# Performance work log

Hardware: AMD Instinct MI355X
Metric: run time of the kernel (lower is better)

The kernel has to match this reference:

```python
import jax, jax.numpy as jnp
import numpy as np

B, S, HID, HEADS = 1, 2048, 4096, 32
HEAD_D = HID // HEADS
SCALE = float(1.0 / np.sqrt(HEAD_D))  # = 1/norm_factor^2 with use_mup=False


def setup_inputs() -> dict:
    key = jax.random.key(0)
    k0, k1, k2, k3, k4 = jax.random.split(key, 5)
    return {
        "x": jax.random.normal(k0, (B, S, HID), jnp.float32),
        "attn_qkvw": jax.random.normal(k1, (HID, 3 * HID), jnp.float32) * 0.02,
        "attn_qkvb": jax.random.normal(k2, (3 * HID,), jnp.float32) * 0.02,
        "attn_ow": jax.random.normal(k3, (HID, HID), jnp.float32) * 0.02,
        "attn_ob": jax.random.normal(k4, (HID,), jnp.float32) * 0.02,
    }


def reference(x, attn_qkvw, attn_qkvb, attn_ow, attn_ob):
    # QKV projection (LinearOp): [B,S,HID] @ [HID,3*HID] + bias -> packed qkv
    qkv = x @ attn_qkvw + attn_qkvb
    q, k, v = jnp.split(qkv, 3, axis=-1)  # each [B,S,HID]

    def to_heads(t):
        return t.reshape(B, S, HEADS, HEAD_D)

    q, k, v = to_heads(q), to_heads(k), to_heads(v)
    # flash kernel math: softmax(scale * q k^T + causal mask) @ v (numerically
    # stable online softmax == standard stable softmax)
    scores = jnp.einsum("bqhd,bkhd->bhqk", q, k) * jnp.float32(SCALE)
    causal = jnp.tril(jnp.ones((S, S), dtype=bool))  # P_SEQ = 0
    scores = jnp.where(causal[None, None], scores, jnp.float32(-jnp.inf))
    attn = jax.nn.softmax(scores, axis=-1)
    ctx = jnp.einsum("bhqk,bkhd->bqhd", attn, v).reshape(B, S, HID)
    # output projection
    return ctx @ attn_ow + attn_ob
```

## Files before the change

kernel.cpp:

```cpp
#include <hip/hip_runtime.h>
#include <hip/hip_bf16.h>
#include <math.h>

typedef __bf16 bf16_t;
typedef __bf16 bf16x8 __attribute__((ext_vector_type(8)));
typedef float f32x4 __attribute__((ext_vector_type(4)));

#define AS1 __attribute__((address_space(1)))
#define AS3 __attribute__((address_space(3)))

static constexpr int S_  = 2048;
static constexpr int HID = 4096;
static constexpr int NH  = 32;
static constexpr int HD  = 128;
static constexpr int N3  = 3 * HID;
static constexpr float SC2 = 0.12751674581f;
static constexpr float THR = 11.0f;

__global__ void cvt_f32_bf16(const float* __restrict__ in, bf16_t* __restrict__ out, int n4) {
  int i = blockIdx.x * blockDim.x + threadIdx.x;
  if (i >= n4) return;
  float4 v = ((const float4*)in)[i];
  union { bf16_t h[4]; short4 s4; } u;
  u.h[0] = (bf16_t)v.x; u.h[1] = (bf16_t)v.y; u.h[2] = (bf16_t)v.z; u.h[3] = (bf16_t)v.w;
  ((short4*)out)[i] = u.s4;
}

__global__ __launch_bounds__(256) void transcvt64(
    const float* __restrict__ in, bf16_t* __restrict__ out, int R, int C) {
  __shared__ float t[64][65];
  const int r0 = blockIdx.y * 64, c0 = blockIdx.x * 64;
  const int tid = threadIdx.x;
  const int rr = tid >> 4, c4 = (tid & 15) * 4;
#pragma unroll
  for (int it = 0; it < 4; ++it) {
    float4 v = *(const float4*)&in[(size_t)(r0 + rr + it * 16) * C + c0 + c4];
    t[rr + it * 16][c4 + 0] = v.x;
    t[rr + it * 16][c4 + 1] = v.y;
    t[rr + it * 16][c4 + 2] = v.z;
    t[rr + it * 16][c4 + 3] = v.w;
  }
  __syncthreads();
  const int cc = tid >> 3, r8 = (tid & 7) * 8;
#pragma unroll
  for (int it = 0; it < 2; ++it) {
    const int c = cc + it * 32;
    bf16x8 w;
#pragma unroll
    for (int j = 0; j < 8; ++j) w[j] = (bf16_t)t[r8 + j][c];
    *(bf16x8*)&out[(size_t)(c0 + c) * R + r0 + r8] = w;
  }
}

__global__ void vtrans(const bf16_t* __restrict__ qkv, bf16_t* __restrict__ vt) {
  __shared__ bf16_t t[32][33];
  int h = blockIdx.z;
  int s0 = blockIdx.x * 32, d0 = blockIdx.y * 32;
  int tx = threadIdx.x, ty = threadIdx.y;
#pragma unroll
  for (int i = 0; i < 32; i += 8)
    t[ty + i][tx] = qkv[(size_t)(s0 + ty + i) * N3 + 2 * HID + h * HD + d0 + tx];
  __syncthreads();
#pragma unroll
  for (int i = 0; i < 32; i += 8)
    vt[(size_t)(h * HD + d0 + ty + i) * S_ + s0 + tx] = t[tx][ty + i];
}

template <bool STG, int VMC>
__device__ __forceinline__ void wstep(
    const char* slot, int aoff, int boff,
    const bf16_t* gA, const bf16_t* gB, int kst, size_t row64,
    char* stgA, char* stgB, f32x4 (&acc)[8][4]) {
  bf16x8 a[8], b[4];
#pragma unroll
  for (int mi = 0; mi < 8; ++mi) a[mi] = *(const bf16x8*)(slot + aoff + mi * 1024);
#pragma unroll
  for (int ni = 0; ni < 4; ++ni) b[ni] = *(const bf16x8*)(slot + 16384 + boff + ni * 1024);
  if constexpr (STG) {
#pragma unroll
    for (int i = 0; i < 4; ++i)
      __builtin_amdgcn_global_load_lds((const AS1 void*)(gA + i * row64 + kst),
                                       (AS3 void*)(stgA + i * 4096), 16, 0, 0);
#pragma unroll
    for (int j = 0; j < 2; ++j)
      __builtin_amdgcn_global_load_lds((const AS1 void*)(gB + j * row64 + kst),
                                       (AS3 void*)(stgB + j * 4096), 16, 0, 0);
  }
  if constexpr (VMC == 6)      asm volatile("s_waitcnt vmcnt(6)" ::: "memory");
  else if constexpr (VMC == 0) asm volatile("s_waitcnt vmcnt(0)" ::: "memory");
  asm volatile("s_waitcnt lgkmcnt(0)" ::: "memory");
  __builtin_amdgcn_s_barrier();
  __builtin_amdgcn_s_setprio(1);
#pragma unroll
  for (int mi = 0; mi < 8; ++mi)
#pragma unroll
    for (int ni = 0; ni < 4; ++ni)
      acc[mi][ni] = __builtin_amdgcn_mfma_f32_16x16x32_bf16(a[mi], b[ni], acc[mi][ni], 0, 0, 0);
  __builtin_amdgcn_s_setprio(0);
}

__global__ __launch_bounds__(256, 2) void gemm_w(
    const bf16_t* __restrict__ A, const bf16_t* __restrict__ BT,
    const float* __restrict__ bias, bf16_t* __restrict__ C,
    int M, int N, int K, int ntiles) {
  extern __shared__ char smem[];
  const int tid = threadIdx.x;
  const int wv = tid >> 6, ln = tid & 63;
  const int lr = ln & 15, lg = ln >> 4;
  const int wm = wv >> 1, wn = wv & 1;

  const int nx = N >> 7;
  const int chunk = ntiles >> 3;

  const int lrow = wv * 16 + (ln >> 2);
  const int lcol = ((ln & 3) << 3) ^ ((ln & 32) >> 1);
  const size_t row64 = (size_t)64 * K;
  const int sw = (lr & 8) << 2;
  const int aoff = (wm * 128 + lr) * 64 + ((lg * 16) ^ sw);
  const int boff = (wn * 64 + lr) * 64 + ((lg * 16) ^ sw);
  const int NT = K >> 5;

  for (int tt = blockIdx.x; tt < ntiles; tt += gridDim.x) {
    const int wg = (tt & 7) * chunk + (tt >> 3);
    const int m0 = (wg / nx) * 256, n0 = (wg % nx) * 128;

    const bf16_t* gA = A + (size_t)(m0 + lrow) * K + lcol;
    const bf16_t* gB = BT + (size_t)(n0 + lrow) * K + lcol;

    f32x4 acc[8][4] = {};

#pragma unroll
    for (int t = 0; t < 2; ++t) {
      char* dA = smem + t * 24576 + wv * 1024;
      char* dB = dA + 16384;
#pragma unroll
      for (int i = 0; i < 4; ++i)
        __builtin_amdgcn_global_load_lds((const AS1 void*)(gA + i * row64 + t * 32),
                                         (AS3 void*)(dA + i * 4096), 16, 0, 0);
#pragma unroll
      for (int j = 0; j < 2; ++j)
        __builtin_amdgcn_global_load_lds((const AS1 void*)(gB + j * row64 + t * 32),
                                         (AS3 void*)(dB + j * 4096), 16, 0, 0);
    }
    asm volatile("s_waitcnt vmcnt(6)" ::: "memory");
    __builtin_amdgcn_s_barrier();

    int slot = 0, nslot = 2;
    int t = 0;
    for (; t < NT - 2; ++t) {
      char* sb = smem + nslot * 24576 + wv * 1024;
      wstep<true, 6>(smem + slot * 24576, aoff, boff, gA, gB, (t + 2) * 32,
                     row64, sb, sb + 16384, acc);
      slot = (slot == 2) ? 0 : slot + 1;
      nslot = (nslot == 2) ? 0 : nslot + 1;
    }
    wstep<false, 0>(smem + slot * 24576, aoff, boff, gA, gB, 0, row64, smem, smem, acc);
    slot = (slot == 2) ? 0 : slot + 1;
    wstep<false, -1>(smem + slot * 24576, aoff, boff, gA, gB, 0, row64, smem, smem, acc);

#pragma unroll
    for (int mi = 0; mi < 8; ++mi)
#pragma unroll
      for (int ni = 0; ni < 4; ++ni) {
        const int col = n0 + wn * 64 + ni * 16 + lr;
        const float bv = bias[col];
#pragma unroll
        for (int i = 0; i < 4; ++i) {
          const int row = m0 + wm * 128 + mi * 16 + lg * 4 + i;
          C[(size_t)row * N + col] = (bf16_t)(acc[mi][ni][i] + bv);
        }
      }
  }
}

template <bool STG, int VMC>
__device__ __forceinline__ void tile_step(
    const char* slot, int aoff, int boff,
    const bf16_t* gA, const bf16_t* gB, int kst, size_t skA,
    char* stg_dst, f32x4 (&acc)[4][4]) {
  bf16x8 a[4], b[4];
#pragma unroll
  for (int mi = 0; mi < 4; ++mi) a[mi] = *(const bf16x8*)(slot + aoff + mi * 1024);
#pragma unroll
  for (int ni = 0; ni < 4; ++ni) b[ni] = *(const bf16x8*)(slot + 16384 + boff + ni * 1024);
  if constexpr (STG) {
    __builtin_amdgcn_global_load_lds((const AS1 void*)(gA + kst), (AS3 void*)(stg_dst), 16, 0, 0);
    __builtin_amdgcn_global_load_lds((const AS1 void*)(gA + skA + kst), (AS3 void*)(stg_dst + 8192), 16, 0, 0);
    __builtin_amdgcn_global_load_lds((const AS1 void*)(gB + kst), (AS3 void*)(stg_dst + 16384), 16, 0, 0);
  }
  if constexpr (VMC == 3)      asm volatile("s_waitcnt vmcnt(3)" ::: "memory");
  else if constexpr (VMC == 0) asm volatile("s_waitcnt vmcnt(0)" ::: "memory");
  asm volatile("s_waitcnt lgkmcnt(0)" ::: "memory");
  __builtin_amdgcn_s_barrier();
  __builtin_amdgcn_s_setprio(1);
#pragma unroll
  for (int mi = 0; mi < 4; ++mi)
#pragma unroll
    for (int ni = 0; ni < 4; ++ni)
      acc[mi][ni] = __builtin_amdgcn_mfma_f32_16x16x32_bf16(a[mi], b[ni], acc[mi][ni], 0, 0, 0);
  __builtin_amdgcn_s_setprio(0);
}

template <typename OutT>
__global__ __launch_bounds__(512, 4) void gemm_p(
    const bf16_t* __restrict__ A, const bf16_t* __restrict__ BT,
    const float* __restrict__ bias, OutT* __restrict__ C,
    int M, int N, int K, int ntiles) {
  extern __shared__ char smem[];
  const int tid = threadIdx.x;
  const int wv = tid >> 6, ln = tid & 63;
  const int lr = ln & 15, lg = ln >> 4;
  const int wm = wv >> 1, wn = wv & 1;

  const int nx = N >> 7;
  const int chunk = ntiles >> 3;

  const int lrow = wv * 16 + (ln >> 2);
  const int lcol = ((ln & 3) << 3) ^ ((ln & 32) >> 1);
  const size_t skA = (size_t)128 * K;
  const int sw = (lr & 8) << 2;
  const int aoff = (wm * 64 + lr) * 64 + ((lg * 16) ^ sw);
  const int boff = (wn * 64 + lr) * 64 + ((lg * 16) ^ sw);
  const int NT = K >> 5;

  for (int tt = blockIdx.x; tt < ntiles; tt += gridDim.x) {
    const int wg = (tt & 7) * chunk + (tt >> 3);
    const int m0 = (wg / nx) * 256, n0 = (wg % nx) * 128;

    const bf16_t* gA = A + (size_t)(m0 + lrow) * K + lcol;
    const bf16_t* gB = BT + (size_t)(n0 + lrow) * K + lcol;

    f32x4 acc[4][4] = {};

#pragma unroll
    for (int t = 0; t < 2; ++t) {
      char* d = smem + t * 24576 + wv * 1024;
      __builtin_amdgcn_global_load_lds((const AS1 void*)(gA + t * 32), (AS3 void*)(d), 16, 0, 0);
      __builtin_amdgcn_global_load_lds((const AS1 void*)(gA + skA + t * 32), (AS3 void*)(d + 8192), 16, 0, 0);
      __builtin_amdgcn_global_load_lds((const AS1 void*)(gB + t * 32), (AS3 void*)(d + 16384), 16, 0, 0);
    }
    asm volatile("s_waitcnt vmcnt(3)" ::: "memory");
    __builtin_amdgcn_s_barrier();

    int slot = 0, nslot = 2;
    int t = 0;
    for (; t < NT - 2; ++t) {
      tile_step<true, 3>(smem + slot * 24576, aoff, boff, gA, gB, (t + 2) * 32,
                         skA, smem + nslot * 24576 + wv * 1024, acc);
      slot = (slot == 2) ? 0 : slot + 1;
      nslot = (nslot == 2) ? 0 : nslot + 1;
    }
    tile_step<false, 0>(smem + slot * 24576, aoff, boff, gA, gB, 0, skA, smem, acc);
    slot = (slot == 2) ? 0 : slot + 1;
    tile_step<false, -1>(smem + slot * 24576, aoff, boff, gA, gB, 0, skA, smem, acc);

#pragma unroll
    for (int mi = 0; mi < 4; ++mi)
#pragma unroll
      for (int ni = 0; ni < 4; ++ni) {
        const int col = n0 + wn * 64 + ni * 16 + lr;
        const float bv = bias[col];
#pragma unroll
        for (int i = 0; i < 4; ++i) {
          const int row = m0 + wm * 64 + mi * 16 + lg * 4 + i;
          C[(size_t)row * N + col] = (OutT)(acc[mi][ni][i] + bv);
        }
      }
  }
}

__global__ __launch_bounds__(256, 2) void attn_fwd(
    const bf16_t* __restrict__ qkv, const bf16_t* __restrict__ vt,
    bf16_t* __restrict__ ctx) {
  __shared__ __align__(16) bf16_t Ks[64][136];
  __shared__ __align__(16) bf16_t Vts[128][72];

  const int tid = threadIdx.x;
  const int wv = tid >> 6, ln = tid & 63;
  bf16_t* Pl = &Ks[0][0] + wv * (32 * 68);

  const int bid = blockIdx.x;
  const int a = bid >> 3;
  const int hsub = a >> 4;
  const int h  = ((bid & 7) << 2) + hsub;
  const int qt = 15 - (((a & 15) + (hsub << 2)) & 15);
  const int q0 = qt * 128;
  const int lr = ln & 15, lg = ln >> 4;
  const int rbase = q0 + 32 * wv;

  bf16x8 qf[2][4];
#pragma unroll
  for (int rg = 0; rg < 2; ++rg)
#pragma unroll
    for (int kk = 0; kk < 4; ++kk) {
      bf16x8 r = *(const bf16x8*)(qkv + (size_t)(rbase + 16 * rg + lr) * N3 + h * HD + kk * 32 + lg * 8);
#pragma unroll
      for (int j = 0; j < 8; ++j) r[j] = (bf16_t)((float)r[j] * SC2);
      qf[rg][kk] = r;
    }

  f32x4 oacc[2][8] = {};
  float mrow[2][4], psum[2][4];
#pragma unroll
  for (int rg = 0; rg < 2; ++rg)
#pragma unroll
    for (int i = 0; i < 4; ++i) { mrow[rg][i] = -INFINITY; psum[rg][i] = 0.f; }

  const int k_r = tid >> 4, k_c = (tid & 15) * 8;
  const int v_r = tid >> 3, v_c = (tid & 7) * 8;
  bf16x8 kr[4], vr[4];

#pragma unroll
  for (int it = 0; it < 4; ++it) {
    kr[it] = *(const bf16x8*)(qkv + (size_t)(k_r + it * 16) * N3 + HID + h * HD + k_c);
    vr[it] = *(const bf16x8*)(vt + (size_t)(h * HD + v_r + it * 32) * S_ + v_c);
  }

  const int ntiles = 2 * qt + 2;
  for (int t = 0; t < ntiles; ++t) {
    const int kv0 = t * 64;
    const int kvn = (t + 1 < ntiles) ? kv0 + 64 : 0;
    __syncthreads();
#pragma unroll
    for (int it = 0; it < 4; ++it) {
      *(bf16x8*)&Ks[k_r + it * 16][k_c] = kr[it];
      *(bf16x8*)&Vts[v_r + it * 32][v_c] = vr[it];
    }
#pragma unroll
    for (int it = 0; it < 4; ++it) {
      kr[it] = *(const bf16x8*)(qkv + (size_t)(kvn + k_r + it * 16) * N3 + HID + h * HD + k_c);
      vr[it] = *(const bf16x8*)(vt + (size_t)(h * HD + v_r + it * 32) * S_ + kvn + v_c);
    }
    __syncthreads();

    f32x4 sacc[2][4] = {};
#pragma unroll
    for (int kk = 0; kk < 4; ++kk)
#pragma unroll
      for (int ni = 0; ni < 4; ++ni) {
        bf16x8 kf = *(const bf16x8*)&Ks[16 * ni + lr][kk * 32 + lg * 8];
        sacc[0][ni] = __builtin_amdgcn_mfma_f32_16x16x32_bf16(qf[0][kk], kf, sacc[0][ni], 0, 0, 0);
        sacc[1][ni] = __builtin_amdgcn_mfma_f32_16x16x32_bf16(qf[1][kk], kf, sacc[1][ni], 0, 0, 0);
      }

    float p[2][4][4];
    float mx[2][4];
    bool grow = false;
#pragma unroll
    for (int rg = 0; rg < 2; ++rg) {
      const bool needmask = (kv0 + 63 > rbase + 16 * rg);
#pragma unroll
      for (int i = 0; i < 4; ++i) {
        const int row = rbase + 16 * rg + lg * 4 + i;
        float m_ = -INFINITY;
#pragma unroll
        for (int ni = 0; ni < 4; ++ni) {
          float s = sacc[rg][ni][i];
          if (needmask && (kv0 + 16 * ni + lr > row)) s = -INFINITY;
          p[rg][ni][i] = s;
          m_ = fmaxf(m_, s);
        }
        m_ = fmaxf(m_, __shfl_xor(m_, 1, 64));
        m_ = fmaxf(m_, __shfl_xor(m_, 2, 64));
        m_ = fmaxf(m_, __shfl_xor(m_, 4, 64));
        m_ = fmaxf(m_, __shfl_xor(m_, 8, 64));
        mx[rg][i] = m_;
        grow |= (m_ > mrow[rg][i] + THR);
      }
    }
    if (__any(grow)) {
#pragma unroll
      for (int rg = 0; rg < 2; ++rg) {
        float alpha[4];
#pragma unroll
        for (int i = 0; i < 4; ++i) {
          const float mn = fmaxf(mrow[rg][i], mx[rg][i]);
          alpha[i] = exp2f(mrow[rg][i] - mn);
          mrow[rg][i] = mn;
          psum[rg][i] *= alpha[i];
        }
#pragma unroll
        for (int nf = 0; nf < 8; ++nf)
#pragma unroll
          for (int i = 0; i < 4; ++i) oacc[rg][nf][i] *= alpha[i];
      }
    }
#pragma unroll
    for (int rg = 0; rg < 2; ++rg)
#pragma unroll
      for (int i = 0; i < 4; ++i) {
        float ps = 0.f;
#pragma unroll
        for (int ni = 0; ni < 4; ++ni) {
          float e = exp2f(p[rg][ni][i] - mrow[rg][i]);
          p[rg][ni][i] = e;
          ps += e;
        }
        psum[rg][i] += ps;
      }

    __syncthreads();

#pragma unroll
    for (int rg = 0; rg < 2; ++rg)
#pragma unroll
      for (int ni = 0; ni < 4; ++ni)
#pragma unroll
        for (int i = 0; i < 4; ++i)
          Pl[(16 * rg + lg * 4 + i) * 68 + 16 * ni + lr] = (bf16_t)p[rg][ni][i];

#pragma unroll
    for (int kk2 = 0; kk2 < 2; ++kk2) {
      bf16x8 pf0 = *(const bf16x8*)&Pl[lr * 68 + kk2 * 32 + lg * 8];
      bf16x8 pf1 = *(const bf16x8*)&Pl[(16 + lr) * 68 + kk2 * 32 + lg * 8];
#pragma unroll
      for (int nf = 0; nf < 8; ++nf) {
        bf16x8 vf = *(const bf16x8*)&Vts[16 * nf + lr][kk2 * 32 + lg * 8];
        oacc[0][nf] = __builtin_amdgcn_mfma_f32_16x16x32_bf16(pf0, vf, oacc[0][nf], 0, 0, 0);
        oacc[1][nf] = __builtin_amdgcn_mfma_f32_16x16x32_bf16(pf1, vf, oacc[1][nf], 0, 0, 0);
      }
    }
  }

#pragma unroll
  for (int rg = 0; rg < 2; ++rg) {
#pragma unroll
    for (int i = 0; i < 4; ++i) {
      float s = psum[rg][i];
      s += __shfl_xor(s, 1, 64);
      s += __shfl_xor(s, 2, 64);
      s += __shfl_xor(s, 4, 64);
      s += __shfl_xor(s, 8, 64);
      psum[rg][i] = 1.f / s;
    }
#pragma unroll
    for (int nf = 0; nf < 8; ++nf)
#pragma unroll
      for (int i = 0; i < 4; ++i) {
        int row = rbase + 16 * rg + lg * 4 + i;
        int col = h * HD + 16 * nf + lr;
        ctx[(size_t)row * HID + col] = (bf16_t)(oacc[rg][nf][i] * psum[rg][i]);
      }
  }
}

extern "C" void kernel_launch(void* const* d_in, const int* in_sizes, int n_in,
                              void* d_out, int out_size, void* d_ws, size_t ws_size,
                              hipStream_t stream) {
  const float* x    = (const float*)d_in[0];
  const float* wqkv = (const float*)d_in[1];
  const float* bqkv = (const float*)d_in[2];
  const float* ow   = (const float*)d_in[3];
  const float* ob   = (const float*)d_in[4];
  float* out = (float*)d_out;

  char* w = (char*)d_ws;
  bf16_t* xb    = (bf16_t*)(w);
  bf16_t* wqkvT = (bf16_t*)(w + (size_t)16777216);
  bf16_t* qkv   = (bf16_t*)(w + (size_t)117440512);
  bf16_t* vt    = (bf16_t*)(w + (size_t)167772160);
  bf16_t* ctx   = (bf16_t*)(w + (size_t)184549376);
  bf16_t* owT   = (bf16_t*)(w + (size_t)201326592);

  (void)in_sizes; (void)n_in; (void)out_size; (void)ws_size;

  cvt_f32_bf16<<<(S_ * HID / 4 + 255) / 256, 256, 0, stream>>>(x, xb, S_ * HID / 4);
  transcvt64<<<dim3(N3 / 64, HID / 64), 256, 0, stream>>>(wqkv, wqkvT, HID, N3);
  transcvt64<<<dim3(HID / 64, HID / 64), 256, 0, stream>>>(ow, owT, HID, HID);
  gemm_w<<<512, 256, 73728, stream>>>(xb, wqkvT, bqkv, qkv, S_, N3, HID,
                                      (S_ / 256) * (N3 / 128));
  vtrans<<<dim3(S_ / 32, HD / 32, NH), dim3(32, 8), 0, stream>>>(qkv, vt);
  attn_fwd<<<(S_ / 128) * NH, 256, 0, stream>>>(qkv, vt, ctx);
  gemm_p<float><<<256, 512, 73728, stream>>>(ctx, owT, ob, out, S_, HID, HID,
                                             (S_ / 256) * (HID / 128));
}
```

Measured before the change: 506.0 us.

## Replace QKV GEMM with 256x256-tile, 8-wave kernel using quadrant-staged pipeline

The QKV projection GEMM moves from a 256x128 tile with 4 waves and a 3-slot K=32 ring to a 256x256 tile with 8 waves. It double-buffers K=64 chunks in 128 KB of LDS, with XOR-swizzled layout and four quadrant MFMA phases interleaved with staged global-to-LDS loads. The larger tile is meant to raise arithmetic intensity and cut global/L2 traffic per FLOP, and the quadrant schedule is meant to overlap loads with MFMA. The cost is much more LDS per block, which allows only one block per CU, and many barriers per iteration, which may add synchronisation stalls.

```diff
diff --git a/kernel.cpp b/kernel.cpp
--- a/kernel.cpp
+++ b/kernel.cpp
@@ -66,40 +66,7 @@
     vt[(size_t)(h * HD + d0 + ty + i) * S_ + s0 + tx] = t[tx][ty + i];
 }
 
-template <bool STG, int VMC>
-__device__ __forceinline__ void wstep(
-    const char* slot, int aoff, int boff,
-    const bf16_t* gA, const bf16_t* gB, int kst, size_t row64,
-    char* stgA, char* stgB, f32x4 (&acc)[8][4]) {
-  bf16x8 a[8], b[4];
-#pragma unroll
-  for (int mi = 0; mi < 8; ++mi) a[mi] = *(const bf16x8*)(slot + aoff + mi * 1024);
-#pragma unroll
-  for (int ni = 0; ni < 4; ++ni) b[ni] = *(const bf16x8*)(slot + 16384 + boff + ni * 1024);
-  if constexpr (STG) {
-#pragma unroll
-    for (int i = 0; i < 4; ++i)
-      __builtin_amdgcn_global_load_lds((const AS1 void*)(gA + i * row64 + kst),
-                                       (AS3 void*)(stgA + i * 4096), 16, 0, 0);
-#pragma unroll
-    for (int j = 0; j < 2; ++j)
-      __builtin_amdgcn_global_load_lds((const AS1 void*)(gB + j * row64 + kst),
-                                       (AS3 void*)(stgB + j * 4096), 16, 0, 0);
-  }
-  if constexpr (VMC == 6)      asm volatile("s_waitcnt vmcnt(6)" ::: "memory");
-  else if constexpr (VMC == 0) asm volatile("s_waitcnt vmcnt(0)" ::: "memory");
-  asm volatile("s_waitcnt lgkmcnt(0)" ::: "memory");
-  __builtin_amdgcn_s_barrier();
-  __builtin_amdgcn_s_setprio(1);
-#pragma unroll
-  for (int mi = 0; mi < 8; ++mi)
-#pragma unroll
-    for (int ni = 0; ni < 4; ++ni)
-      acc[mi][ni] = __builtin_amdgcn_mfma_f32_16x16x32_bf16(a[mi], b[ni], acc[mi][ni], 0, 0, 0);
-  __builtin_amdgcn_s_setprio(0);
-}
-
-__global__ __launch_bounds__(256, 2) void gemm_w(
+__global__ __launch_bounds__(512, 2) void gemm256(
     const bf16_t* __restrict__ A, const bf16_t* __restrict__ BT,
     const float* __restrict__ bias, bf16_t* __restrict__ C,
     int M, int N, int K, int ntiles) {
@@ -107,56 +74,121 @@
   const int tid = threadIdx.x;
   const int wv = tid >> 6, ln = tid & 63;
   const int lr = ln & 15, lg = ln >> 4;
-  const int wm = wv >> 1, wn = wv & 1;
-
-  const int nx = N >> 7;
+  const int wm = wv >> 2, wn = wv & 3;
+  const int nx = N >> 8;
   const int chunk = ntiles >> 3;
-
-  const int lrow = wv * 16 + (ln >> 2);
-  const int lcol = ((ln & 3) << 3) ^ ((ln & 32) >> 1);
-  const size_t row64 = (size_t)64 * K;
-  const int sw = (lr & 8) << 2;
-  const int aoff = (wm * 128 + lr) * 64 + ((lg * 16) ^ sw);
-  const int boff = (wn * 64 + lr) * 64 + ((lg * 16) ^ sw);
-  const int NT = K >> 5;
+  (void)M;
+
+  const int srow = tid >> 3;
+  const int scol = 8 * ((tid & 7) ^ (srow & 7));
+  const int xorb = (lr & 7) << 4;
+  const int abase = wm * 16384 + lr * 128;
+  const int bbase = 32768 + (wn >> 1) * 16384 + ((wn & 1) * 64 + lr) * 128;
+  const int NI = K >> 7;
+
+#define VMC(n) asm volatile("s_waitcnt vmcnt(" #n ")" ::: "memory")
+#define LGKM0() asm volatile("s_waitcnt lgkmcnt(0)" ::: "memory")
+#define BAR() __builtin_amdgcn_s_barrier()
+#define QUAD(AH, BP)                                                                 \
+  __builtin_amdgcn_s_setprio(1);                                                     \
+  _Pragma("unroll") for (int q = 0; q < 4; ++q)                                      \
+  _Pragma("unroll") for (int r = 0; r < 2; ++r)                                      \
+  _Pragma("unroll") for (int kk = 0; kk < 2; ++kk)                                   \
+      acc[(AH) * 4 + q][(BP) * 2 + r] = __builtin_amdgcn_mfma_f32_16x16x32_bf16(     \
+          a[q][kk], b[r][kk], acc[(AH) * 4 + q][(BP) * 2 + r], 0, 0, 0);             \
+  __builtin_amdgcn_s_setprio(0)
 
   for (int tt = blockIdx.x; tt < ntiles; tt += gridDim.x) {
     const int wg = (tt & 7) * chunk + (tt >> 3);
-    const int m0 = (wg / nx) * 256, n0 = (wg % nx) * 128;
-
-    const bf16_t* gA = A + (size_t)(m0 + lrow) * K + lcol;
-    const bf16_t* gB = BT + (size_t)(n0 + lrow) * K + lcol;
+    const int m0 = (wg / nx) * 256, n0 = (wg % nx) * 256;
+
+    const bf16_t* gA = A + (size_t)(m0 + srow) * K + scol;
+    const bf16_t* gB = BT + (size_t)(n0 + srow) * K + scol;
+
+    auto STG = [&](int H, int t) {
+      const bf16_t* src = ((H < 2) ? gA : gB) + (size_t)((H & 1) * 128) * K + t * 64;
+      char* dst = smem + (t & 1) * 65536 + H * 16384 + tid * 16;
+      __builtin_amdgcn_global_load_lds((const AS1 void*)src, (AS3 void*)dst, 16, 0, 0);
+      __builtin_amdgcn_global_load_lds((const AS1 void*)(src + (size_t)64 * K),
+                                       (AS3 void*)(dst + 8192), 16, 0, 0);
+    };
+    auto LDA = [&](int c, int mi, int kk) {
+      return *(const bf16x8*)(smem + c * 65536 + abase + mi * 2048 +
+                              ((kk * 64 + lg * 16) ^ xorb));
+    };
+    auto LDB = [&](int c, int ni, int kk) {
+      return *(const bf16x8*)(smem + c * 65536 + bbase + ni * 2048 +
+                              ((kk * 64 + lg * 16) ^ xorb));
+    };
 
     f32x4 acc[8][4] = {};
 
-#pragma unroll
-    for (int t = 0; t < 2; ++t) {
-      char* dA = smem + t * 24576 + wv * 1024;
-      char* dB = dA + 16384;
-#pragma unroll
-      for (int i = 0; i < 4; ++i)
-        __builtin_amdgcn_global_load_lds((const AS1 void*)(gA + i * row64 + t * 32),
-                                         (AS3 void*)(dA + i * 4096), 16, 0, 0);
-#pragma unroll
-      for (int j = 0; j < 2; ++j)
-        __builtin_amdgcn_global_load_lds((const AS1 void*)(gB + j * row64 + t * 32),
-                                         (AS3 void*)(dB + j * 4096), 16, 0, 0);
-    }
-    asm volatile("s_waitcnt vmcnt(6)" ::: "memory");
-    __builtin_amdgcn_s_barrier();
-
-    int slot = 0, nslot = 2;
-    int t = 0;
-    for (; t < NT - 2; ++t) {
-      char* sb = smem + nslot * 24576 + wv * 1024;
-      wstep<true, 6>(smem + slot * 24576, aoff, boff, gA, gB, (t + 2) * 32,
-                     row64, sb, sb + 16384, acc);
-      slot = (slot == 2) ? 0 : slot + 1;
-      nslot = (nslot == 2) ? 0 : nslot + 1;
-    }
-    wstep<false, 0>(smem + slot * 24576, aoff, boff, gA, gB, 0, row64, smem, smem, acc);
-    slot = (slot == 2) ? 0 : slot + 1;
-    wstep<false, -1>(smem + slot * 24576, aoff, boff, gA, gB, 0, row64, smem, smem, acc);
+    STG(0, 0); STG(1, 0); STG(2, 0); STG(3, 0);
+    STG(0, 1);
+    VMC(2);
+    BAR();
+
+    for (int j = 0; j < NI; ++j) {
+      const int t1 = 2 * j + 1;
+      const bool md = (j != NI - 1);
+      bf16x8 a[4][2], b[2][2];
+
+      STG(1, t1);
+      VMC(4);
+      BAR();
+#pragma unroll
+      for (int q = 0; q < 4; ++q) { a[q][0] = LDA(0, q, 0); a[q][1] = LDA(0, q, 1); }
+#pragma unroll
+      for (int r = 0; r < 2; ++r) { b[r][0] = LDB(0, r, 0); b[r][1] = LDB(0, r, 1); }
+      LGKM0();
+      QUAD(0, 0);
+      BAR();
+#pragma unroll
+      for (int r = 0; r < 2; ++r) { b[r][0] = LDB(0, 2 + r, 0); b[r][1] = LDB(0, 2 + r, 1); }
+      STG(2, t1);
+      BAR(); LGKM0();
+      QUAD(0, 1);
+      BAR();
+#pragma unroll
+      for (int q = 0; q < 4; ++q) { a[q][0] = LDA(0, 4 + q, 0); a[q][1] = LDA(0, 4 + q, 1); }
+      STG(3, t1);
+      BAR(); LGKM0();
+      QUAD(1, 1);
+      BAR();
+#pragma unroll
+      for (int r = 0; r < 2; ++r) { b[r][0] = LDB(0, r, 0); b[r][1] = LDB(0, r, 1); }
+      if (md) STG(0, 2 * j + 2);
+      BAR(); LGKM0();
+      QUAD(1, 0);
+      BAR();
+      if (md) { STG(1, 2 * j + 2); VMC(4); } else { VMC(0); }
+      BAR();
+#pragma unroll
+      for (int q = 0; q < 4; ++q) { a[q][0] = LDA(1, q, 0); a[q][1] = LDA(1, q, 1); }
+#pragma unroll
+      for (int r = 0; r < 2; ++r) { b[r][0] = LDB(1, r, 0); b[r][1] = LDB(1, r, 1); }
+      LGKM0();
+      QUAD(0, 0);
+      BAR();
+#pragma unroll
+      for (int r = 0; r < 2; ++r) { b[r][0] = LDB(1, 2 + r, 0); b[r][1] = LDB(1, 2 + r, 1); }
+      if (md) STG(2, 2 * j + 2);
+      BAR(); LGKM0();
+      QUAD(0, 1);
+      BAR();
+#pragma unroll
+      for (int q = 0; q < 4; ++q) { a[q][0] = LDA(1, 4 + q, 0); a[q][1] = LDA(1, 4 + q, 1); }
+      if (md) STG(3, 2 * j + 2);
+      BAR(); LGKM0();
+      QUAD(1, 1);
+      BAR();
+#pragma unroll
+      for (int r = 0; r < 2; ++r) { b[r][0] = LDB(1, r, 0); b[r][1] = LDB(1, r, 1); }
+      if (md) STG(0, 2 * j + 3);
+      BAR(); LGKM0();
+      QUAD(1, 0);
+      BAR();
+    }
 
 #pragma unroll
     for (int mi = 0; mi < 8; ++mi)
@@ -171,6 +203,10 @@
         }
       }
   }
+#undef VMC
+#undef LGKM0
+#undef BAR
+#undef QUAD
 }
 
 template <bool STG, int VMC>
@@ -467,8 +503,8 @@
   cvt_f32_bf16<<<(S_ * HID / 4 + 255) / 256, 256, 0, stream>>>(x, xb, S_ * HID / 4);
   transcvt64<<<dim3(N3 / 64, HID / 64), 256, 0, stream>>>(wqkv, wqkvT, HID, N3);
   transcvt64<<<dim3(HID / 64, HID / 64), 256, 0, stream>>>(ow, owT, HID, HID);
-  gemm_w<<<512, 256, 73728, stream>>>(xb, wqkvT, bqkv, qkv, S_, N3, HID,
-                                      (S_ / 256) * (N3 / 128));
+  gemm256<<<256, 512, 131072, stream>>>(xb, wqkvT, bqkv, qkv, S_, N3, HID,
+                                        (S_ / 256) * (N3 / 256));
   vtrans<<<dim3(S_ / 32, HD / 32, NH), dim3(32, 8), 0, stream>>>(qkv, vt);
   attn_fwd<<<(S_ / 128) * NH, 256, 0, stream>>>(qkv, vt, ctx);
   gemm_p<float><<<256, 512, 73728, stream>>>(ctx, owT, ob, out, S_, HID, HID,
```

New measurement: 503.7 us. No clear change (-0.4%).
